# Kernel tuning notes

Hardware: AMD Instinct MI355X
Metric: run time of the kernel (lower is better)

## Reference

```python
import jax, jax.numpy as jnp
import numpy as np

N_NODES = 100000
N_EDGES = 1600000
D_IN = 128
D_OUT = 128
ALPHA = 0.01   # LeakyReLU negative slope
BN_EPS = 1e-5


def setup_inputs() -> dict:
    key = jax.random.key(0)
    ks = jax.random.split(key, 4)
    x = jax.random.normal(ks[0], (N_NODES, D_IN), dtype=jnp.float32)
    edge_idx = jax.random.randint(ks[1], (2, N_EDGES), 0, N_NODES, dtype=jnp.int64)
    # SAGEConv params: lin_l (neighbor path, with bias) and lin_r (root path, no bias)
    s = 1.0 / np.sqrt(D_IN)
    W_l = jax.random.uniform(ks[2], (D_OUT, D_IN), jnp.float32, -s, s)
    b_l = jnp.zeros((D_OUT,), jnp.float32)
    W_r = jax.random.uniform(ks[3], (D_OUT, D_IN), jnp.float32, -s, s)
    gamma = jnp.ones((D_OUT,), jnp.float32)
    beta = jnp.zeros((D_OUT,), jnp.float32)
    return {"x": x, "edge_idx": edge_idx, "W_l": W_l, "b_l": b_l,
            "W_r": W_r, "gamma": gamma, "beta": beta}


def reference(x, edge_idx, W_l, b_l, W_r, gamma, beta):
    src = edge_idx[0]
    dst = edge_idx[1]
    # mean aggregation of source-node features at target nodes (PyG SAGEConv default)
    msg_sum = jax.ops.segment_sum(x[src], dst, num_segments=N_NODES)      # [N, D_IN]
    cnt = jax.ops.segment_sum(jnp.ones((src.shape[0],), x.dtype), dst,
                              num_segments=N_NODES)                        # [N]
    mean = msg_sum / jnp.maximum(cnt, 1.0)[:, None]
    # out = lin_l(mean_agg) + lin_r(x)
    h = mean @ W_l.T + b_l + x @ W_r.T                                     # [N, D_OUT]
    # BatchNorm1d in training mode (biased variance over node dim)
    mu = jnp.mean(h, axis=0)
    var = jnp.mean((h - mu) ** 2, axis=0)
    h = gamma * (h - mu) * jax.lax.rsqrt(var + BN_EPS) + beta
    # LeakyReLU
    return jnp.where(h >= 0, h, ALPHA * h)
```

## Files before the change

kernel.cpp:

```cpp
#include <hip/hip_runtime.h>
#include <hip/hip_bf16.h>
#include <stdint.h>

#define N_NODES 100000
#define N_EDGES 1600000
#define DIM     128
#define ALPHA   0.01f
#define BN_EPS  1e-5f
#define NBUCK   3125
#define NBLK_P  256
#define EPB     6250
#define SRT_CAP 1536
#define GEMM_GRID 391

typedef __bf16 bf16x8 __attribute__((ext_vector_type(8)));
typedef float  f32x4  __attribute__((ext_vector_type(4)));
typedef float  f32x2  __attribute__((ext_vector_type(2)));

#if defined(__has_builtin)
#if __has_builtin(__builtin_amdgcn_cvt_pk_fp8_f32) && __has_builtin(__builtin_amdgcn_cvt_pk_f32_fp8)
#define USE_FP8_BUILTIN 1
#endif
#endif

static const size_t OFF_SUM   = 512;
static const size_t OFF_SUMSQ = 1024;
static const size_t OFF_BBASE = 2048;
static const size_t OFF_BT    = 14592;
static const size_t OFF_TMP   = 32768;
static const size_t OFF_BFRAG = 6432768;
static const size_t OFF_AMEAN = 6498304;
static const size_t OFF_X8    = 32098304;
static const size_t OFF_H     = 44898304;
static const size_t OFF_GHIST = OFF_H;
static const size_t OFF_SOFFT = OFF_H + 4194304;
static const size_t OFF_XB    = 70498304;

__device__ __forceinline__ float bf2f(unsigned short h) {
    return __uint_as_float(((unsigned int)h) << 16);
}
__device__ __forceinline__ float bflo(unsigned int w) {
    return __uint_as_float(w << 16);
}
__device__ __forceinline__ float bfhi(unsigned int w) {
    return __uint_as_float(w & 0xffff0000u);
}
__device__ __forceinline__ unsigned short f2bf(float f) {
    unsigned int u = __float_as_uint(f);
    u = u + 0x7fffu + ((u >> 16) & 1u);
    return (unsigned short)(u >> 16);
}
__device__ __forceinline__ unsigned int pack2(float a, float b) {
    return (unsigned int)f2bf(a) | ((unsigned int)f2bf(b) << 16);
}
__device__ __forceinline__ float loadS(const void* p, int i, int isf32) {
    return isf32 ? ((const float*)p)[i] : bf2f(((const unsigned short*)p)[i]);
}
__device__ __forceinline__ int edge_at(const void* e, long long i, int idx64) {
    return idx64 ? (int)((const long long*)e)[i] : ((const int*)e)[i];
}
__device__ __forceinline__ int blkpos(int k) { return ((k & 7) << 5) | (k >> 3); }
__device__ __forceinline__ int posblk(int p) { return ((p & 31) << 3) | (p >> 5); }

__device__ __forceinline__ void gload_lds16(const void* g, void* l) {
    __builtin_amdgcn_global_load_lds(
        reinterpret_cast<const __attribute__((address_space(1))) unsigned int*>(
            reinterpret_cast<uintptr_t>(g)),
        reinterpret_cast<__attribute__((address_space(3))) unsigned int*>(
            reinterpret_cast<uintptr_t>(l)),
        16, 0, 0);
}

#ifndef USE_FP8_BUILTIN
__device__ __forceinline__ unsigned int enc_fp8_1(float f) {
    unsigned int u = __float_as_uint(f);
    unsigned int s = (u >> 24) & 0x80u;
    unsigned int au = u & 0x7fffffffu;
    if (au >= 0x43E00000u) return s | 0x7Eu;
    if (au < 0x3C800000u) {
        int m = (int)rintf(__uint_as_float(au) * 512.0f);
        return s | (unsigned int)m;
    }
    unsigned int r = au + 0x7FFFFu + ((au >> 20) & 1u);
    unsigned int e = (r >> 23) & 0xffu;
    unsigned int m3 = (r >> 20) & 7u;
    return s | ((e - 120u) << 3) | m3;
}
#endif
__device__ __forceinline__ unsigned int enc4(float f0, float f1, float f2, float f3) {
#ifdef USE_FP8_BUILTIN
    int r = __builtin_amdgcn_cvt_pk_fp8_f32(f0, f1, 0, false);
    r = __builtin_amdgcn_cvt_pk_fp8_f32(f2, f3, r, true);
    return (unsigned int)r;
#else
    return enc_fp8_1(f0) | (enc_fp8_1(f1) << 8) | (enc_fp8_1(f2) << 16) | (enc_fp8_1(f3) << 24);
#endif
}
__device__ __forceinline__ void dec4(unsigned int w, float* o) {
#ifdef USE_FP8_BUILTIN
    f32x2 a = __builtin_amdgcn_cvt_pk_f32_fp8(w, false);
    f32x2 b = __builtin_amdgcn_cvt_pk_f32_fp8(w, true);
    o[0] = a[0]; o[1] = a[1]; o[2] = b[0]; o[3] = b[1];
#else
    #pragma unroll
    for (int j = 0; j < 4; j++) {
        unsigned int c = (w >> (8 * j)) & 0xffu;
        o[j] = __uint_as_float(((c & 0x80u) << 24) | ((c & 0x7fu) << 20)) * 0x1p120f;
    }
#endif
}

__device__ __forceinline__ int detect_idx64(const void* e) {
    const unsigned int* ew = (const unsigned int*)e;
    unsigned long long m = __ballot(ew[2 * (threadIdx.x & 63) + 1] != 0u);
    return (__popcll(m) < 8) ? 1 : 0;
}
__device__ __forceinline__ int detect_isf32(const void* x) {
    const unsigned int* xw = (const unsigned int*)x;
    unsigned int w = xw[threadIdx.x & 63];
    unsigned int e = (w >> 7) & 0xffu;
    bool bflike = (e >= 110u && e <= 140u) || ((w & 0xffffu) == 0u);
    unsigned long long m = __ballot(bflike);
    return (__popcll(m) > 32) ? 0 : 1;
}

__global__ __launch_bounds__(256) void k1_kernel(const void* edges, const void* x,
                                                 int* ghist, unsigned int* x8,
                                                 unsigned short* xb, float* gz) {
    int tid = threadIdx.x;
    if (blockIdx.x < NBLK_P) {
        __shared__ int sh[NBUCK];
        int idx64 = detect_idx64(edges);
        int blk = blockIdx.x;
        if (blk == 0) gz[tid] = 0.f;
        for (int i = tid; i < NBUCK; i += 256) sh[i] = 0;
        __syncthreads();
        long long base = (long long)blk * EPB;
        for (int i = tid; i < EPB; i += 256) {
            int d = edge_at(edges, (long long)N_EDGES + base + i, idx64);
            atomicAdd(&sh[d >> 5], 1);
        }
        __syncthreads();
        for (int i = tid; i < NBUCK; i += 256) ghist[blk * NBUCK + i] = sh[i];
    } else {
        int isf32 = detect_isf32(x);
        int gid = (blockIdx.x - NBLK_P) * 256 + tid;
        float f[16];
        if (!isf32) {
            const uint4* xv = (const uint4*)x;
            uint4 a = xv[gid * 2], b2 = xv[gid * 2 + 1];
            unsigned int w[8] = {a.x, a.y, a.z, a.w, b2.x, b2.y, b2.z, b2.w};
            #pragma unroll
            for (int i = 0; i < 8; i++) { f[2 * i] = bflo(w[i]); f[2 * i + 1] = bfhi(w[i]); }
        } else {
            const float4* xf = (const float4*)x;
            #pragma unroll
            for (int i = 0; i < 4; i++) {
                float4 v = xf[gid * 4 + i];
                f[4 * i] = v.x; f[4 * i + 1] = v.y; f[4 * i + 2] = v.z; f[4 * i + 3] = v.w;
            }
            uint4 h1, h2;
            h1.x = pack2(f[0], f[1]);  h1.y = pack2(f[2], f[3]);
            h1.z = pack2(f[4], f[5]);  h1.w = pack2(f[6], f[7]);
            h2.x = pack2(f[8], f[9]);  h2.y = pack2(f[10], f[11]);
            h2.z = pack2(f[12], f[13]); h2.w = pack2(f[14], f[15]);
            ((uint4*)xb)[gid * 2]     = h1;
            ((uint4*)xb)[gid * 2 + 1] = h2;
        }
        uint4 o;
        o.x = enc4(f[0], f[1], f[2], f[3]);
        o.y = enc4(f[4], f[5], f[6], f[7]);
        o.z = enc4(f[8], f[9], f[10], f[11]);
        o.w = enc4(f[12], f[13], f[14], f[15]);
        *(uint4*)(x8 + gid * 4) = o;
    }
}

__global__ __launch_bounds__(64) void p2a_kernel(const int* __restrict__ ghist,
                                                 int* __restrict__ sOffT,
                                                 int* __restrict__ bT) {
    int b = blockIdx.x * 64 + threadIdx.x;
    if (b >= NBUCK) return;
    int run = 0;
    #pragma unroll 8
    for (int p = 0; p < NBLK_P; p++) {
        int k = posblk(p);
        int v = ghist[k * NBUCK + b];
        sOffT[p * NBUCK + b] = run;
        run += v;
    }
    bT[b] = run;
}

__global__ __launch_bounds__(256) void k3_kernel(const int* bT, int* bucketBase,
                                                 const void* W_l, const void* W_r,
                                                 const void* x, unsigned short* bfrag) {
    int t = threadIdx.x;
    if (blockIdx.x == 0) {
        __shared__ int ws[4];
        int base = t * 13;
        int v[13]; int s = 0;
        #pragma unroll
        for (int i = 0; i < 13; i++) {
            int idx = base + i;
            v[i] = (idx < NBUCK) ? bT[idx] : 0;
            s += v[i];
        }
        int lane = t & 63, wv = t >> 6;
        int sc = s;
        #pragma unroll
        for (int off = 1; off < 64; off <<= 1) {
            int u = __shfl_up(sc, off, 64);
            if (lane >= off) sc += u;
        }
        if (lane == 63) ws[wv] = sc;
        __syncthreads();
        int add = 0;
        for (int w = 0; w < wv; w++) add += ws[w];
        int run = sc - s + add;
        #pragma unroll
        for (int i = 0; i < 13; i++) {
            int idx = base + i;
            if (idx < NBUCK) bucketBase[idx] = run;
            run += v[i];
        }
    } else {
        int isf32 = detect_isf32(x);
        int g = (blockIdx.x - 1) * 256 + t;
        int j    = g & 7;
        int lane = (g >> 3) & 63;
        int s    = (g >> 9) & 7;
        int tt   = (g >> 12) & 7;
        int n = tt * 16 + (lane & 15);
        int k = s * 32 + ((lane >> 4) & 3) * 8 + j;
        float v = (k < DIM) ? loadS(W_l, n * DIM + k, isf32)
                            : loadS(W_r, n * DIM + (k - DIM), isf32);
        bfrag[g] = f2bf(v);
    }
}

__global__ __launch_bounds__(1024) void p3_kernel(const void* edges, const int* __restrict__ sOffT,
                                                  const int* __restrict__ bucketBase,
                                                  unsigned int* __restrict__ tmp) {
    __shared__ int sbase[NBUCK];
    int idx64 = detect_idx64(edges);
    int blk = blockIdx.x, tid = threadIdx.x;
    int mypos = blkpos(blk);
    for (int i = tid; i < NBUCK; i += 1024)
        sbase[i] = bucketBase[i] + sOffT[(size_t)mypos * NBUCK + i];
    __syncthreads();
    long long base = (long long)blk * EPB;
    for (int i = tid; i < EPB; i += 1024) {
        long long e = base + i;
        int s = edge_at(edges, e, idx64);
        int d = edge_at(edges, (long long)N_EDGES + e, idx64);
        int p = atomicAdd(&sbase[d >> 5], 1);
        tmp[p] = ((unsigned int)(d & 31) << 17) | (unsigned int)s;
    }
}

__global__ __launch_bounds__(256) void agg_kernel(const unsigned int* x8, const unsigned int* tmp,
                                                  const int* bucketBase, unsigned short* Amean) {
    __shared__ int s_cnt[32];
    __shared__ int s_beg[32];
    __shared__ int s_srt[SRT_CAP];
    int b = blockIdx.x, tid = threadIdx.x;
    int gb = bucketBase[b];
    int ge = (b == NBUCK - 1) ? N_EDGES : bucketBase[b + 1];
    int nE = min(ge - gb, SRT_CAP);
    if (tid < 32) s_cnt[tid] = 0;
    __syncthreads();
    for (int i = tid; i < nE; i += 256) atomicAdd(&s_cnt[tmp[gb + i] >> 17], 1);
    __syncthreads();
    if (tid < 32) {
        int v = s_cnt[tid];
        int sc = v;
        #pragma unroll
        for (int off = 1; off < 32; off <<= 1) {
            int u = __shfl_up(sc, off, 64);
            if (tid >= off) sc += u;
        }
        s_beg[tid] = sc - v;
        s_cnt[tid] = sc - v;
    }
    __syncthreads();
    for (int i = tid; i < nE; i += 256) {
        unsigned int w = tmp[gb + i];
        int p = atomicAdd(&s_cnt[w >> 17], 1);
        s_srt[p] = (int)(w & 0x1ffffu);
    }
    __syncthreads();
    int wv = tid >> 6, lane = tid & 63;
    int oct = lane >> 3, l8 = lane & 7;
    int nl = wv * 8 + oct;
    int nb = s_beg[nl], ne2 = s_cnt[nl];
    const uint4* xv = (const uint4*)x8;
    float acc[16];
    #pragma unroll
    for (int i = 0; i < 16; i++) acc[i] = 0.f;
    for (int jj = nb; jj < ne2; jj += 4) {
        uint4 r[4]; float mk[4];
        #pragma unroll
        for (int u = 0; u < 4; u++) {
            int e = jj + u;
            int su = s_srt[(e < ne2) ? e : nb];
            mk[u] = (e < ne2) ? 1.f : 0.f;
            r[u] = xv[(size_t)su * 8 + l8];
        }
        #pragma unroll
        for (int u = 0; u < 4; u++) {
            float f[4];
            dec4(r[u].x, f);
            acc[0] = fmaf(f[0], mk[u], acc[0]);  acc[1] = fmaf(f[1], mk[u], acc[1]);
            acc[2] = fmaf(f[2], mk[u], acc[2]);  acc[3] = fmaf(f[3], mk[u], acc[3]);
            dec4(r[u].y, f);
            acc[4] = fmaf(f[0], mk[u], acc[4]);  acc[5] = fmaf(f[1], mk[u], acc[5]);
            acc[6] = fmaf(f[2], mk[u], acc[6]);  acc[7] = fmaf(f[3], mk[u], acc[7]);
            dec4(r[u].z, f);
            acc[8] = fmaf(f[0], mk[u], acc[8]);  acc[9] = fmaf(f[1], mk[u], acc[9]);
            acc[10] = fmaf(f[2], mk[u], acc[10]); acc[11] = fmaf(f[3], mk[u], acc[11]);
            dec4(r[u].w, f);
            acc[12] = fmaf(f[0], mk[u], acc[12]); acc[13] = fmaf(f[1], mk[u], acc[13]);
            acc[14] = fmaf(f[2], mk[u], acc[14]); acc[15] = fmaf(f[3], mk[u], acc[15]);
        }
    }
    int ng = b * 32 + nl;
    float inv = 1.0f / (float)max(ne2 - nb, 1);
    uint4 o1, o2;
    o1.x = pack2(acc[0] * inv, acc[1] * inv);
    o1.y = pack2(acc[2] * inv, acc[3] * inv);
    o1.z = pack2(acc[4] * inv, acc[5] * inv);
    o1.w = pack2(acc[6] * inv, acc[7] * inv);
    o2.x = pack2(acc[8] * inv, acc[9] * inv);
    o2.y = pack2(acc[10] * inv, acc[11] * inv);
    o2.z = pack2(acc[12] * inv, acc[13] * inv);
    o2.w = pack2(acc[14] * inv, acc[15] * inv);
    *(uint4*)(Amean + (size_t)ng * 128 + l8 * 16) = o1;
    *(uint4*)(Amean + (size_t)ng * 128 + l8 * 16 + 8) = o2;
}

__global__ __launch_bounds__(256, 2) void gemm_kernel(const unsigned short* __restrict__ Amean,
                                                      const void* __restrict__ x,
                                                      const unsigned short* __restrict__ xb,
                                                      const unsigned short* __restrict__ Bfrag_g,
                                                      const void* __restrict__ b_l,
                                                      unsigned int* __restrict__ Hu,
                                                      float* __restrict__ gpart) {
    __shared__ unsigned short lds[32768];
    __shared__ float sstat[2][128];
    int isf32 = detect_isf32(x);
    const unsigned short* xs = isf32 ? xb : (const unsigned short*)x;
    int tid = threadIdx.x;
    int wave = tid >> 6, lane = tid & 63;
    int lm = lane & 15, lq = lane >> 4;

    #pragma unroll
    for (int k = 0; k < 16; k++) {
        int e = tid + k * 256;
        gload_lds16(Bfrag_g + (size_t)e * 8, lds + (size_t)e * 8);
    }
    if (tid < 128) { sstat[0][tid] = 0.f; sstat[1][tid] = 0.f; }

    int base = blockIdx.x * 256;
    bf16x8 aq[4][8];
    #pragma unroll
    for (int j = 0; j < 4; j++) {
        int rowA = base + (wave * 4 + j) * 16 + lm;
        if (rowA >= N_NODES) rowA = N_NODES - 1;
        const unsigned short* am = Amean + (size_t)rowA * 128 + lq * 8;
        const unsigned short* xm = xs + (size_t)rowA * 128 + lq * 8;
        #pragma unroll
        for (int s = 0; s < 4; s++) aq[j][s] = *(const bf16x8*)(am + s * 32);
        #pragma unroll
        for (int s = 0; s < 4; s++) aq[j][4 + s] = *(const bf16x8*)(xm + s * 32);
    }
    float bv[8];
    #pragma unroll
    for (int t = 0; t < 8; t++) bv[t] = loadS(b_l, t * 16 + lm, isf32);
    float st1[8], st2[8];
    #pragma unroll
    for (int t = 0; t < 8; t++) { st1[t] = 0.f; st2[t] = 0.f; }

    __syncthreads();

    #pragma unroll
    for (int j = 0; j < 4; j++) {
        f32x4 acc[8];
        #pragma unroll
        for (int t = 0; t < 8; t++) acc[t] = (f32x4){0.f, 0.f, 0.f, 0.f};
        #pragma unroll
        for (int s = 0; s < 8; s++) {
            #pragma unroll
            for (int t = 0; t < 8; t++) {
                bf16x8 bb = *(const bf16x8*)(lds + ((t * 8 + s) * 64 + lane) * 8);
                acc[t] = __builtin_amdgcn_mfma_f32_16x16x32_bf16(aq[j][s], bb, acc[t], 0, 0, 0);
            }
        }
        #pragma unroll
        for (int t = 0; t < 8; t++) {
            #pragma unroll
            for (int r = 0; r < 4; r++) {
                int ro = base + (wave * 4 + j) * 16 + lq * 4 + r;
                float v = acc[t][r] + bv[t];
                float p = __shfl_xor(v, 1, 64);
                bool in = (ro < N_NODES);
                if (in) { st1[t] += v; st2[t] += v * v; }
                if (in && !(lm & 1)) Hu[(size_t)ro * 64 + t * 8 + (lm >> 1)] = pack2(v, p);
            }
        }
    }
    #pragma unroll
    for (int t = 0; t < 8; t++) {
        atomicAdd(&sstat[0][t * 16 + lm], st1[t]);
        atomicAdd(&sstat[1][t * 16 + lm], st2[t]);
    }
    __syncthreads();
    gpart[(size_t)blockIdx.x * 256 + threadIdx.x] = ((const float*)sstat)[threadIdx.x];
}

__global__ __launch_bounds__(256) void redux_kernel(const float* gpart, float* gz) {
    int t = threadIdx.x;
    float a = 0.f;
    for (int b = blockIdx.x; b < GEMM_GRID; b += 8)
        a += gpart[(size_t)b * 256 + t];
    atomicAdd(&gz[t], a);
}

__global__ __launch_bounds__(256) void bn_norm_kernel(const unsigned int* __restrict__ Hu,
                                                      const void* x,
                                                      const float* gsum,
                                                      const float* gsumsq, const void* gamma,
                                                      const void* beta, void* out) {
    __shared__ float sc[128], sh[128];
    int isf32 = detect_isf32(x);
    int tid = threadIdx.x;
    if (tid < 128) {
        const float invN = 1.0f / (float)N_NODES;
        float mu = gsum[tid] * invN;
        float var = gsumsq[tid] * invN - mu * mu;
        float rstd = rsqrtf(var + BN_EPS);
        float g = loadS(gamma, tid, isf32);
        float b = loadS(beta, tid, isf32);
        sc[tid] = g * rstd;
        sh[tid] = b - mu * g * rstd;
    }
    __syncthreads();
    size_t idx = (size_t)blockIdx.x * 256 + tid;
    size_t i8 = idx * 8;
    float h[8];
    {
        uint4 u = *(const uint4*)(Hu + idx * 4);
        h[0]=bflo(u.x); h[1]=bfhi(u.x); h[2]=bflo(u.y); h[3]=bfhi(u.y);
        h[4]=bflo(u.z); h[5]=bfhi(u.z); h[6]=bflo(u.w); h[7]=bfhi(u.w);
    }
    int c0 = (int)(i8 & 127);
    float o[8];
    #pragma unroll
    for (int i = 0; i < 8; i++) {
        float v = h[i] * sc[c0 + i] + sh[c0 + i];
        o[i] = (v >= 0.f) ? v : ALPHA * v;
    }
    if (isf32) {
        *(float4*)((float*)out + i8) = make_float4(o[0], o[1], o[2], o[3]);
        *(float4*)((float*)out + i8 + 4) = make_float4(o[4], o[5], o[6], o[7]);
    } else {
        uint4 u;
        u.x = pack2(o[0], o[1]); u.y = pack2(o[2], o[3]);
        u.z = pack2(o[4], o[5]); u.w = pack2(o[6], o[7]);
        *(uint4*)((unsigned short*)out + i8) = u;
    }
}

extern "C" void kernel_launch(void* const* d_in, const int* in_sizes, int n_in,
                              void* d_out, int out_size, void* d_ws, size_t ws_size,
                              hipStream_t stream) {
    const void* x     = d_in[0];
    const void* eidx  = d_in[1];
    const void* W_l   = d_in[2];
    const void* b_l   = d_in[3];
    const void* W_r   = d_in[4];
    const void* gamma = d_in[5];
    const void* beta  = d_in[6];
    char* ws = (char*)d_ws;
    float* gsum = (float*)(ws + OFF_SUM);
    float* gsumsq = (float*)(ws + OFF_SUMSQ);
    int* bucketBase = (int*)(ws + OFF_BBASE);
    int* bT = (int*)(ws + OFF_BT);
    unsigned int* tmp = (unsigned int*)(ws + OFF_TMP);
    unsigned short* bfrag = (unsigned short*)(ws + OFF_BFRAG);
    unsigned short* Amean = (unsigned short*)(ws + OFF_AMEAN);
    unsigned int* x8 = (unsigned int*)(ws + OFF_X8);
    unsigned int* H = (unsigned int*)(ws + OFF_H);
    unsigned short* xb = (unsigned short*)(ws + OFF_XB);
    int* ghist = (int*)(ws + OFF_GHIST);
    int* sOffT = (int*)(ws + OFF_SOFFT);
    float* gpart = (float*)(ws + OFF_TMP);

    k1_kernel<<<NBLK_P + 3125, 256, 0, stream>>>(eidx, x, ghist, x8, xb, gsum);
    p2a_kernel<<<49, 64, 0, stream>>>(ghist, sOffT, bT);
    k3_kernel<<<129, 256, 0, stream>>>(bT, bucketBase, W_l, W_r, x, bfrag);
    p3_kernel<<<NBLK_P, 1024, 0, stream>>>(eidx, sOffT, bucketBase, tmp);
    agg_kernel<<<NBUCK, 256, 0, stream>>>(x8, tmp, bucketBase, Amean);
    gemm_kernel<<<GEMM_GRID, 256, 0, stream>>>(Amean, x, xb, bfrag, b_l, H, gpart);
    redux_kernel<<<8, 256, 0, stream>>>(gpart, gsum);
    bn_norm_kernel<<<6250, 256, 0, stream>>>(H, x, gsum, gsumsq, gamma, beta, d_out);
}
```

Before: 254.2 us.

## Fuse BN stats reduction and normalization into GEMM via grid barrier

```diff
diff --git a/kernel.cpp b/kernel.cpp
--- a/kernel.cpp
+++ b/kernel.cpp
@@ -24,16 +24,15 @@
 #endif
 
 static const size_t OFF_SUM   = 512;
-static const size_t OFF_SUMSQ = 1024;
 static const size_t OFF_BBASE = 2048;
 static const size_t OFF_BT    = 14592;
 static const size_t OFF_TMP   = 32768;
 static const size_t OFF_BFRAG = 6432768;
 static const size_t OFF_AMEAN = 6498304;
 static const size_t OFF_X8    = 32098304;
-static const size_t OFF_H     = 44898304;
-static const size_t OFF_GHIST = OFF_H;
-static const size_t OFF_SOFFT = OFF_H + 4194304;
+static const size_t OFF_SPARE = 44898304;
+static const size_t OFF_GHIST = OFF_SPARE;
+static const size_t OFF_SOFFT = OFF_SPARE + 4194304;
 static const size_t OFF_XB    = 70498304;
 
 __device__ __forceinline__ float bf2f(unsigned short h) {
@@ -132,7 +131,10 @@
         __shared__ int sh[NBUCK];
         int idx64 = detect_idx64(edges);
         int blk = blockIdx.x;
-        if (blk == 0) gz[tid] = 0.f;
+        if (blk == 0) {
+            gz[tid] = 0.f;
+            if (tid == 0) ((int*)gz)[256] = 0;
+        }
         for (int i = tid; i < NBUCK; i += 256) sh[i] = 0;
         __syncthreads();
         long long base = (long long)blk * EPB;
@@ -176,20 +178,27 @@
     }
 }
 
-__global__ __launch_bounds__(64) void p2a_kernel(const int* __restrict__ ghist,
-                                                 int* __restrict__ sOffT,
-                                                 int* __restrict__ bT) {
-    int b = blockIdx.x * 64 + threadIdx.x;
-    if (b >= NBUCK) return;
-    int run = 0;
-    #pragma unroll 8
-    for (int p = 0; p < NBLK_P; p++) {
-        int k = posblk(p);
-        int v = ghist[k * NBUCK + b];
-        sOffT[p * NBUCK + b] = run;
-        run += v;
-    }
-    bT[b] = run;
+__global__ __launch_bounds__(512) void p2a_kernel(const int* __restrict__ ghist,
+                                                  int* __restrict__ sOffT,
+                                                  int* __restrict__ bT) {
+    __shared__ int csum[8][64];
+    int t = threadIdx.x;
+    int c = t >> 6, bl = t & 63;
+    int b = blockIdx.x * 64 + bl;
+    int v[32]; int s = 0;
+    if (b < NBUCK) {
+        #pragma unroll
+        for (int i = 0; i < 32; i++) { v[i] = ghist[(size_t)(i * 8 + c) * NBUCK + b]; s += v[i]; }
+    }
+    csum[c][bl] = s;
+    __syncthreads();
+    if (b < NBUCK) {
+        int run = 0;
+        for (int i = 0; i < c; i++) run += csum[i][bl];
+        #pragma unroll
+        for (int i = 0; i < 32; i++) { sOffT[(size_t)(c * 32 + i) * NBUCK + b] = run; run += v[i]; }
+        if (c == 7) bT[b] = run;
+    }
 }
 
 __global__ __launch_bounds__(256) void k3_kernel(const int* bT, int* bucketBase,
@@ -344,10 +353,15 @@
                                                       const unsigned short* __restrict__ xb,
                                                       const unsigned short* __restrict__ Bfrag_g,
                                                       const void* __restrict__ b_l,
-                                                      unsigned int* __restrict__ Hu,
-                                                      float* __restrict__ gpart) {
+                                                      const void* __restrict__ gamma,
+                                                      const void* __restrict__ beta,
+                                                      float* __restrict__ gz,
+                                                      void* __restrict__ out) {
     __shared__ unsigned short lds[32768];
     __shared__ float sstat[2][128];
+    float* gsum = gz;
+    float* gsumsq = gz + 128;
+    int* cnt = (int*)(gz + 256);
     int isf32 = detect_isf32(x);
     const unsigned short* xs = isf32 ? xb : (const unsigned short*)x;
     int tid = threadIdx.x;
@@ -383,17 +397,17 @@
 
     __syncthreads();
 
+    f32x4 acc[4][8];
     #pragma unroll
     for (int j = 0; j < 4; j++) {
-        f32x4 acc[8];
-        #pragma unroll
-        for (int t = 0; t < 8; t++) acc[t] = (f32x4){0.f, 0.f, 0.f, 0.f};
+        #pragma unroll
+        for (int t = 0; t < 8; t++) acc[j][t] = (f32x4){0.f, 0.f, 0.f, 0.f};
         #pragma unroll
         for (int s = 0; s < 8; s++) {
             #pragma unroll
             for (int t = 0; t < 8; t++) {
                 bf16x8 bb = *(const bf16x8*)(lds + ((t * 8 + s) * 64 + lane) * 8);
-                acc[t] = __builtin_amdgcn_mfma_f32_16x16x32_bf16(aq[j][s], bb, acc[t], 0, 0, 0);
+                acc[j][t] = __builtin_amdgcn_mfma_f32_16x16x32_bf16(aq[j][s], bb, acc[j][t], 0, 0, 0);
             }
         }
         #pragma unroll
@@ -401,11 +415,10 @@
             #pragma unroll
             for (int r = 0; r < 4; r++) {
                 int ro = base + (wave * 4 + j) * 16 + lq * 4 + r;
-                float v = acc[t][r] + bv[t];
-                float p = __shfl_xor(v, 1, 64);
-                bool in = (ro < N_NODES);
-                if (in) { st1[t] += v; st2[t] += v * v; }
-                if (in && !(lm & 1)) Hu[(size_t)ro * 64 + t * 8 + (lm >> 1)] = pack2(v, p);
+                if (ro < N_NODES) {
+                    float v = acc[j][t][r] + bv[t];
+                    st1[t] += v; st2[t] += v * v;
+                }
             }
         }
     }
@@ -415,59 +428,53 @@
         atomicAdd(&sstat[1][t * 16 + lm], st2[t]);
     }
     __syncthreads();
-    gpart[(size_t)blockIdx.x * 256 + threadIdx.x] = ((const float*)sstat)[threadIdx.x];
-}
-
-__global__ __launch_bounds__(256) void redux_kernel(const float* gpart, float* gz) {
-    int t = threadIdx.x;
-    float a = 0.f;
-    for (int b = blockIdx.x; b < GEMM_GRID; b += 8)
-        a += gpart[(size_t)b * 256 + t];
-    atomicAdd(&gz[t], a);
-}
-
-__global__ __launch_bounds__(256) void bn_norm_kernel(const unsigned int* __restrict__ Hu,
-                                                      const void* x,
-                                                      const float* gsum,
-                                                      const float* gsumsq, const void* gamma,
-                                                      const void* beta, void* out) {
-    __shared__ float sc[128], sh[128];
-    int isf32 = detect_isf32(x);
-    int tid = threadIdx.x;
+    if (tid < 128) {
+        atomicAdd(&gsum[tid], sstat[0][tid]);
+        atomicAdd(&gsumsq[tid], sstat[1][tid]);
+    }
+    __syncthreads();
+    if (tid == 0) {
+        __threadfence();
+        __hip_atomic_fetch_add(cnt, 1, __ATOMIC_ACQ_REL, __HIP_MEMORY_SCOPE_AGENT);
+        while (__hip_atomic_load(cnt, __ATOMIC_ACQUIRE, __HIP_MEMORY_SCOPE_AGENT) < GEMM_GRID)
+            __builtin_amdgcn_s_sleep(8);
+    }
+    __syncthreads();
+    float* scsh = (float*)lds;
     if (tid < 128) {
         const float invN = 1.0f / (float)N_NODES;
-        float mu = gsum[tid] * invN;
-        float var = gsumsq[tid] * invN - mu * mu;
+        float mu = __hip_atomic_load(&gsum[tid], __ATOMIC_RELAXED, __HIP_MEMORY_SCOPE_AGENT) * invN;
+        float m2 = __hip_atomic_load(&gsumsq[tid], __ATOMIC_RELAXED, __HIP_MEMORY_SCOPE_AGENT) * invN;
+        float var = m2 - mu * mu;
         float rstd = rsqrtf(var + BN_EPS);
         float g = loadS(gamma, tid, isf32);
         float b = loadS(beta, tid, isf32);
-        sc[tid] = g * rstd;
-        sh[tid] = b - mu * g * rstd;
-    }
-    __syncthreads();
-    size_t idx = (size_t)blockIdx.x * 256 + tid;
-    size_t i8 = idx * 8;
-    float h[8];
-    {
-        uint4 u = *(const uint4*)(Hu + idx * 4);
-        h[0]=bflo(u.x); h[1]=bfhi(u.x); h[2]=bflo(u.y); h[3]=bfhi(u.y);
-        h[4]=bflo(u.z); h[5]=bfhi(u.z); h[6]=bflo(u.w); h[7]=bfhi(u.w);
-    }
-    int c0 = (int)(i8 & 127);
-    float o[8];
-    #pragma unroll
-    for (int i = 0; i < 8; i++) {
-        float v = h[i] * sc[c0 + i] + sh[c0 + i];
-        o[i] = (v >= 0.f) ? v : ALPHA * v;
-    }
-    if (isf32) {
-        *(float4*)((float*)out + i8) = make_float4(o[0], o[1], o[2], o[3]);
-        *(float4*)((float*)out + i8 + 4) = make_float4(o[4], o[5], o[6], o[7]);
-    } else {
-        uint4 u;
-        u.x = pack2(o[0], o[1]); u.y = pack2(o[2], o[3]);
-        u.z = pack2(o[4], o[5]); u.w = pack2(o[6], o[7]);
-        *(uint4*)((unsigned short*)out + i8) = u;
+        scsh[tid] = g * rstd;
+        scsh[128 + tid] = b - mu * g * rstd;
+    }
+    __syncthreads();
+    float* outf = (float*)out;
+    unsigned int* outu = (unsigned int*)out;
+    #pragma unroll
+    for (int t = 0; t < 8; t++) {
+        int col = t * 16 + lm;
+        float sc = scsh[col], sh = scsh[128 + col];
+        #pragma unroll
+        for (int j = 0; j < 4; j++) {
+            #pragma unroll
+            for (int r = 0; r < 4; r++) {
+                int ro = base + (wave * 4 + j) * 16 + lq * 4 + r;
+                float v = (acc[j][t][r] + bv[t]) * sc + sh;
+                v = (v >= 0.f) ? v : ALPHA * v;
+                float p = __shfl_xor(v, 1, 64);
+                bool in = (ro < N_NODES);
+                if (isf32) {
+                    if (in) outf[(size_t)ro * 128 + col] = v;
+                } else {
+                    if (in && !(lm & 1)) outu[(size_t)ro * 64 + t * 8 + (lm >> 1)] = pack2(v, p);
+                }
+            }
+        }
     }
 }
 
@@ -482,26 +489,21 @@
     const void* gamma = d_in[5];
     const void* beta  = d_in[6];
     char* ws = (char*)d_ws;
-    float* gsum = (float*)(ws + OFF_SUM);
-    float* gsumsq = (float*)(ws + OFF_SUMSQ);
+    float* gz = (float*)(ws + OFF_SUM);
     int* bucketBase = (int*)(ws + OFF_BBASE);
     int* bT = (int*)(ws + OFF_BT);
     unsigned int* tmp = (unsigned int*)(ws + OFF_TMP);
     unsigned short* bfrag = (unsigned short*)(ws + OFF_BFRAG);
     unsigned short* Amean = (unsigned short*)(ws + OFF_AMEAN);
     unsigned int* x8 = (unsigned int*)(ws + OFF_X8);
-    unsigned int* H = (unsigned int*)(ws + OFF_H);
     unsigned short* xb = (unsigned short*)(ws + OFF_XB);
     int* ghist = (int*)(ws + OFF_GHIST);
     int* sOffT = (int*)(ws + OFF_SOFFT);
-    float* gpart = (float*)(ws + OFF_TMP);
-
-    k1_kernel<<<NBLK_P + 3125, 256, 0, stream>>>(eidx, x, ghist, x8, xb, gsum);
-    p2a_kernel<<<49, 64, 0, stream>>>(ghist, sOffT, bT);
+
+    k1_kernel<<<NBLK_P + 3125, 256, 0, stream>>>(eidx, x, ghist, x8, xb, gz);
+    p2a_kernel<<<49, 512, 0, stream>>>(ghist, sOffT, bT);
     k3_kernel<<<129, 256, 0, stream>>>(bT, bucketBase, W_l, W_r, x, bfrag);
     p3_kernel<<<NBLK_P, 1024, 0, stream>>>(eidx, sOffT, bucketBase, tmp);
     agg_kernel<<<NBUCK, 256, 0, stream>>>(x8, tmp, bucketBase, Amean);
-    gemm_kernel<<<GEMM_GRID, 256, 0, stream>>>(Amean, x, xb, bfrag, b_l, H, gpart);
-    redux_kernel<<<8, 256, 0, stream>>>(gpart, gsum);
-    bn_norm_kernel<<<6250, 256, 0, stream>>>(H, x, gsum, gsumsq, gamma, beta, d_out);
-}
+    gemm_kernel<<<GEMM_GRID, 256, 0, stream>>>(Amean, x, xb, bfrag, b_l, gamma, beta, gz, d_out);
+}
```

Measured after the change: 377.8 us. +48.6%, slower.
